# Kernel optimization log

Measured on AMD Instinct MI355X. Metric: run time of the kernel, lower is better.

Reference implementation:

```python
import jax, jax.numpy as jnp
import numpy as np

B, N, C, H = 4, 1024, 1024, 16
HD = C // H
SCALE = HD ** -0.5


def _init_linear(key, out_dim, in_dim):
    # torch nn.Linear default init: U(-1/sqrt(in), 1/sqrt(in)) for weight and bias
    kw, kb = jax.random.split(key)
    bound = 1.0 / np.sqrt(in_dim)
    W = jax.random.uniform(kw, (out_dim, in_dim), jnp.float32, -bound, bound)
    b = jax.random.uniform(kb, (out_dim,), jnp.float32, -bound, bound)
    return W, b


def setup_inputs() -> dict:
    key = jax.random.key(0)
    ks = jax.random.split(key, 5)
    x = jax.random.normal(ks[0], (B, N, C), jnp.float32)
    # NdLinear qkv: Linear(N->N) along seq axis, then Linear(C->3C) along channel axis
    Wq0, bq0 = _init_linear(ks[1], N, N)
    Wq1, bq1 = _init_linear(ks[2], 3 * C, C)
    # NdLinear proj: Linear(N->N) along seq axis, then Linear(C->C) along channel axis
    Wp0, bp0 = _init_linear(ks[3], N, N)
    Wp1, bp1 = _init_linear(ks[4], C, C)
    return {"x": x, "Wq0": Wq0, "bq0": bq0, "Wq1": Wq1, "bq1": bq1,
            "Wp0": Wp0, "bp0": bp0, "Wp1": Wp1, "bp1": bp1}


def _ndlinear(x, W0, b0, W1, b1):
    # NdLinear over (seq, channel): apply Linear along axis 1, then axis 2.
    # torch Linear: y = x @ W.T + b
    x = jnp.einsum('bnc,mn->bmc', x, W0) + b0[None, :, None]   # seq axis
    x = jnp.einsum('bnc,dc->bnd', x, W1) + b1                  # channel axis
    return x


def reference(x, Wq0, bq0, Wq1, bq1, Wp0, bp0, Wp1, bp1):
    qkv = _ndlinear(x, Wq0, bq0, Wq1, bq1)                     # (B, N, 3C)
    qkv = qkv.reshape(B, N, 3, H, HD).transpose(2, 0, 3, 1, 4) # (3, B, H, N, HD)
    q, k, v = qkv[0], qkv[1], qkv[2]
    attn = jnp.einsum('bhnd,bhmd->bhnm', q, k) * SCALE         # (B, H, N, N)
    attn = jax.nn.softmax(attn, axis=-1)
    out = jnp.einsum('bhnm,bhmd->bhnd', attn, v)               # (B, H, N, HD)
    out = out.transpose(0, 2, 1, 3).reshape(B, N, C)
    out = _ndlinear(out, Wp0, bp0, Wp1, bp1)
    return out
```

## Files before the change

kernel.cpp:

```cpp
#include <hip/hip_runtime.h>
#include <hip/hip_bf16.h>
#include <stdint.h>

typedef __bf16 bf16;
typedef __bf16 bf16x4 __attribute__((ext_vector_type(4)));
typedef __bf16 bf16x8 __attribute__((ext_vector_type(8)));
typedef float f32x4 __attribute__((ext_vector_type(4)));

#define B_ 4
#define N_ 1024
#define C_ 1024
#define H_ 16
#define MEG (1u << 20)

__device__ __forceinline__ uint32_t lds_off(const void* p) {
    return (uint32_t)(uintptr_t)p;
}
__device__ __forceinline__ void g2l16(const void* g, uint32_t lds_byte) {
    __builtin_amdgcn_global_load_lds(
        (const __attribute__((address_space(1))) unsigned int*)(uintptr_t)g,
        (__attribute__((address_space(3))) unsigned int*)(uintptr_t)lds_byte,
        16, 0, 0);
}

__global__ __launch_bounds__(256) void prep_k(
    const float* __restrict__ x, bf16* __restrict__ xT,
    const float* __restrict__ s0, bf16* __restrict__ d0,
    const float* __restrict__ s1, bf16* __restrict__ d1,
    const float* __restrict__ s2, bf16* __restrict__ d2,
    const float* __restrict__ s3, bf16* __restrict__ d3)
{
    __shared__ bf16 t[64][66];
    const int bid = blockIdx.x;
    const int tid = threadIdx.x;
    if (bid < 3072) {
        const float* s; bf16* d; int base;
        if (bid < 512)       { s = s0; d = d0; base = 0; }
        else if (bid < 2048) { s = s1; d = d1; base = 512; }
        else if (bid < 2560) { s = s2; d = d2; base = 2048; }
        else                 { s = s3; d = d3; base = 2560; }
        int i = ((bid - base) * 256 + tid) * 8;
        float4 a = *(const float4*)(s + i);
        float4 b = *(const float4*)(s + i + 4);
        bf16x8 r;
        r[0] = (bf16)a.x; r[1] = (bf16)a.y; r[2] = (bf16)a.z; r[3] = (bf16)a.w;
        r[4] = (bf16)b.x; r[5] = (bf16)b.y; r[6] = (bf16)b.z; r[7] = (bf16)b.w;
        *(bf16x8*)(d + i) = r;
        return;
    }
    const int idx = bid - 3072;
    const int c0 = (idx & 15) * 64, n0 = ((idx >> 4) & 15) * 64, b = idx >> 8;
    {
        int nl = tid >> 2, seg = tid & 3;
        const float* src = x + ((size_t)b * N_ + n0 + nl) * C_ + c0 + seg * 16;
#pragma unroll
        for (int i = 0; i < 4; ++i) {
            float4 v = *(const float4*)(src + i * 4);
            t[nl][seg * 16 + i * 4 + 0] = (bf16)v.x;
            t[nl][seg * 16 + i * 4 + 1] = (bf16)v.y;
            t[nl][seg * 16 + i * 4 + 2] = (bf16)v.z;
            t[nl][seg * 16 + i * 4 + 3] = (bf16)v.w;
        }
    }
    __syncthreads();
    {
        int cl = tid >> 2, seg = tid & 3;
        bf16* dst = xT + ((size_t)b * C_ + c0 + cl) * N_ + n0 + seg * 16;
        bf16x8 o0, o1;
#pragma unroll
        for (int j = 0; j < 8; ++j) o0[j] = t[seg * 16 + j][cl];
#pragma unroll
        for (int j = 0; j < 8; ++j) o1[j] = t[seg * 16 + 8 + j][cl];
        *(bf16x8*)dst = o0;
        *(bf16x8*)(dst + 8) = o1;
    }
}

template <int BIAS, bool OF32, bool VSPLIT>
__global__ __launch_bounds__(512) void gemm_k(
    const bf16* __restrict__ A, const bf16* __restrict__ Bm,
    const float* __restrict__ bias, void* __restrict__ Cv,
    bf16* __restrict__ vT,
    int M, int Nn, int K, long long sA, long long sB, long long sC)
{
    __shared__ bf16 smem[2][2][128 * 64];

    const int tid = threadIdx.x;
    const int lane = tid & 63, wid = tid >> 6;
    const int lr = lane & 15, lg = lane >> 4;
    const int wr = wid >> 2, wc = wid & 3;
    const int m0 = blockIdx.y * 128, n0 = blockIdx.x * 128;

    const bf16* Ab = A + (size_t)blockIdx.z * sA;
    const bf16* Bb = Bm + (size_t)blockIdx.z * sB;

    const uint32_t a_lds0 = lds_off(&smem[0][0][0]);
    const uint32_t b_lds0 = lds_off(&smem[0][1][0]);
    const uint32_t bufstride = 2 * 128 * 64 * 2;

    auto stage = [&](int kt, int buf) {
#pragma unroll
        for (int half = 0; half < 2; ++half) {
            int it = tid + half * 512;
            int r = it >> 3, ch = it & 7;
            int sch = ch ^ (r & 7);
            g2l16(Ab + (size_t)(m0 + r) * K + kt * 64 + sch * 8,
                  a_lds0 + buf * bufstride + it * 16);
            g2l16(Bb + (size_t)(n0 + r) * K + kt * 64 + sch * 8,
                  b_lds0 + buf * bufstride + it * 16);
        }
    };

    f32x4 acc[4][2];
#pragma unroll
    for (int i = 0; i < 4; ++i)
#pragma unroll
        for (int j = 0; j < 2; ++j) { f32x4 z = {0.f,0.f,0.f,0.f}; acc[i][j] = z; }

    stage(0, 0);
    __syncthreads();

    const int nt = K >> 6;
    for (int t = 0; t < nt; ++t) {
        int buf = t & 1;
        if (t + 1 < nt) stage(t + 1, buf ^ 1);
        const bf16* As = &smem[buf][0][0];
        const bf16* Bs = &smem[buf][1][0];
#pragma unroll
        for (int s = 0; s < 2; ++s) {
            bf16x8 af[4], bfr[2];
#pragma unroll
            for (int mi = 0; mi < 4; ++mi) {
                int row = wr * 64 + mi * 16 + lr;
                int slot = (s * 4 + lg) ^ (row & 7);
                af[mi] = *(const bf16x8*)(As + row * 64 + slot * 8);
            }
#pragma unroll
            for (int ni = 0; ni < 2; ++ni) {
                int row = wc * 32 + ni * 16 + lr;
                int slot = (s * 4 + lg) ^ (row & 7);
                bfr[ni] = *(const bf16x8*)(Bs + row * 64 + slot * 8);
            }
#pragma unroll
            for (int mi = 0; mi < 4; ++mi)
#pragma unroll
                for (int ni = 0; ni < 2; ++ni)
                    acc[mi][ni] = __builtin_amdgcn_mfma_f32_16x16x32_bf16(
                        af[mi], bfr[ni], acc[mi][ni], 0, 0, 0);
        }
        __syncthreads();
    }

#pragma unroll
    for (int mi = 0; mi < 4; ++mi)
#pragma unroll
        for (int ni = 0; ni < 2; ++ni) {
            int col = n0 + wc * 32 + ni * 16 + lr;
            if constexpr (VSPLIT) {
                if (col >= 2048) {
                    float bv = bias[col];
                    bf16x4 w;
#pragma unroll
                    for (int r = 0; r < 4; ++r) w[r] = (bf16)(acc[mi][ni][r] + bv);
                    int row0 = m0 + wr * 64 + mi * 16 + lg * 4;
                    int bb = row0 >> 10, n = row0 & 1023;
                    *(bf16x4*)(vT + (size_t)bb * MEG +
                               (size_t)(col - 2048) * 1024 + n) = w;
                    continue;
                }
            }
#pragma unroll
            for (int r = 0; r < 4; ++r) {
                int row = m0 + wr * 64 + mi * 16 + lg * 4 + r;
                float bv = (BIAS == 0) ? bias[row] : bias[col];
                float v = acc[mi][ni][r] + bv;
                if constexpr (OF32)
                    ((float*)Cv + (size_t)blockIdx.z * sC)[(size_t)row * Nn + col] = v;
                else
                    ((bf16*)Cv + (size_t)blockIdx.z * sC)[(size_t)row * Nn + col] = (bf16)v;
            }
        }
}

template <int BIAS, bool OF32>
__global__ __launch_bounds__(256) void gemm64_k(
    const bf16* __restrict__ A, const bf16* __restrict__ Bm,
    const float* __restrict__ bias, void* __restrict__ Cv,
    int M, int Nn, int K, long long sA, long long sB, long long sC)
{
    __shared__ bf16 smem[2][192 * 64];

    const int tid = threadIdx.x;
    const int lane = tid & 63, wid = tid >> 6;
    const int lr = lane & 15, lg = lane >> 4;
    const int wr = wid >> 1, wc = wid & 1;
    const int m0 = blockIdx.y * 128, n0 = blockIdx.x * 64;

    const bf16* Ab = A + (size_t)blockIdx.z * sA;
    const bf16* Bb = Bm + (size_t)blockIdx.z * sB;

    const uint32_t a_lds0 = lds_off(&smem[0][0]);
    const uint32_t b_lds0 = a_lds0 + 128 * 64 * 2;
    const uint32_t bufstride = 192 * 64 * 2;

    auto stage = [&](int kt, int buf) {
#pragma unroll
        for (int h = 0; h < 4; ++h) {
            int it = tid + h * 256;
            int r = it >> 3, ch = it & 7;
            int sch = ch ^ (r & 7);
            g2l16(Ab + (size_t)(m0 + r) * K + kt * 64 + sch * 8,
                  a_lds0 + buf * bufstride + it * 16);
        }
#pragma unroll
        for (int h = 0; h < 2; ++h) {
            int it = tid + h * 256;
            int r = it >> 3, ch = it & 7;
            int sch = ch ^ (r & 7);
            g2l16(Bb + (size_t)(n0 + r) * K + kt * 64 + sch * 8,
                  b_lds0 + buf * bufstride + it * 16);
        }
    };

    f32x4 acc[4][2];
#pragma unroll
    for (int i = 0; i < 4; ++i)
#pragma unroll
        for (int j = 0; j < 2; ++j) { f32x4 z = {0.f,0.f,0.f,0.f}; acc[i][j] = z; }

    stage(0, 0);
    __syncthreads();

    const int nt = K >> 6;
    for (int t = 0; t < nt; ++t) {
        int buf = t & 1;
        if (t + 1 < nt) stage(t + 1, buf ^ 1);
        const bf16* As = &smem[buf][0];
        const bf16* Bs = &smem[buf][128 * 64];
#pragma unroll
        for (int s = 0; s < 2; ++s) {
            bf16x8 af[4], bfr[2];
#pragma unroll
            for (int mi = 0; mi < 4; ++mi) {
                int row = wr * 64 + mi * 16 + lr;
                int slot = (s * 4 + lg) ^ (row & 7);
                af[mi] = *(const bf16x8*)(As + row * 64 + slot * 8);
            }
#pragma unroll
            for (int ni = 0; ni < 2; ++ni) {
                int row = wc * 32 + ni * 16 + lr;
                int slot = (s * 4 + lg) ^ (row & 7);
                bfr[ni] = *(const bf16x8*)(Bs + row * 64 + slot * 8);
            }
#pragma unroll
            for (int mi = 0; mi < 4; ++mi)
#pragma unroll
                for (int ni = 0; ni < 2; ++ni)
                    acc[mi][ni] = __builtin_amdgcn_mfma_f32_16x16x32_bf16(
                        af[mi], bfr[ni], acc[mi][ni], 0, 0, 0);
        }
        __syncthreads();
    }

#pragma unroll
    for (int mi = 0; mi < 4; ++mi)
#pragma unroll
        for (int ni = 0; ni < 2; ++ni)
#pragma unroll
            for (int r = 0; r < 4; ++r) {
                int row = m0 + wr * 64 + mi * 16 + lg * 4 + r;
                int col = n0 + wc * 32 + ni * 16 + lr;
                float bv = (BIAS == 0) ? bias[row] : bias[col];
                float v = acc[mi][ni][r] + bv;
                if constexpr (OF32)
                    ((float*)Cv + (size_t)blockIdx.z * sC)[(size_t)row * Nn + col] = v;
                else
                    ((bf16*)Cv + (size_t)blockIdx.z * sC)[(size_t)row * Nn + col] = (bf16)v;
            }
}

__global__ __launch_bounds__(256) void attn_k(
    const bf16* __restrict__ qkv, const bf16* __restrict__ vT,
    bf16* __restrict__ aoT)
{
    __shared__ bf16 Ks[2][4096];
    __shared__ bf16 Vs[2][4096];
    __shared__ bf16 pbuf[4][2048];

    const int tid = threadIdx.x;
    const int lane = tid & 63, wid = tid >> 6;
    const int lr = lane & 15, lg = lane >> 4;
    const int bid = blockIdx.x;
    const int qt = bid >> 6, hb = bid & 63;
    const int b = hb >> 4, h = hb & 15;
    const int qrow0 = qt * 128 + wid * 32;
    const int hoff = h * 64;
    const bf16* qkvb = qkv + (size_t)b * (N_ * 3 * C_);
    const bf16* vTb  = vT + (size_t)b * MEG;

    bf16x8 qfA[2], qfB[2];
#pragma unroll
    for (int kk = 0; kk < 2; ++kk) {
        qfA[kk] = *(const bf16x8*)(qkvb + (size_t)(qrow0 + lr) * 3072 +
                                   hoff + kk * 32 + lg * 8);
        qfB[kk] = *(const bf16x8*)(qkvb + (size_t)(qrow0 + 16 + lr) * 3072 +
                                   hoff + kk * 32 + lg * 8);
#pragma unroll
        for (int j = 0; j < 8; ++j) {
            qfA[kk][j] = (bf16)((float)qfA[kk][j] * 0.18033688f);
            qfB[kk][j] = (bf16)((float)qfB[kk][j] * 0.18033688f);
        }
    }

    const uint32_t ks0 = lds_off(&Ks[0][0]);
    const uint32_t vs0 = lds_off(&Vs[0][0]);

    auto stageK = [&](int kt, int buf) {
#pragma unroll
        for (int hh = 0; hh < 2; ++hh) {
            int it = tid + hh * 256;
            int key = it >> 3, ch = it & 7;
            int sch = ch ^ (key & 7);
            g2l16(qkvb + (size_t)(kt * 64 + key) * 3072 + C_ + hoff + sch * 8,
                  ks0 + buf * 8192 + it * 16);
        }
    };
    auto stageV = [&](int kt, int buf) {
#pragma unroll
        for (int hh = 0; hh < 2; ++hh) {
            int it = tid + hh * 256;
            int d = it >> 3, ch = it & 7;
            int sch = ch ^ (d & 7);
            g2l16(vTb + (size_t)(hoff + d) * 1024 + kt * 64 + sch * 8,
                  vs0 + buf * 8192 + it * 16);
        }
    };

    float lsumA = 0.f, lsumB = 0.f;
    f32x4 oA[4], oB[4];
#pragma unroll
    for (int i = 0; i < 4; ++i) {
        f32x4 z = {0.f,0.f,0.f,0.f};
        oA[i] = z; oB[i] = z;
    }

    char* prowA = (char*)&pbuf[wid][0] + lr * 128;
    char* prowB = (char*)&pbuf[wid][0] + (16 + lr) * 128;
    const int swz = (lr & 7) << 4;

    stageK(0, 0);
    stageV(0, 0);
    __syncthreads();

    for (int kt = 0; kt < 16; ++kt) {
        int buf = kt & 1;
        if (kt + 1 < 16) {
            stageK(kt + 1, buf ^ 1);
            stageV(kt + 1, buf ^ 1);
        }

        f32x4 sA[4], sB[4];
        __builtin_amdgcn_s_setprio(1);
#pragma unroll
        for (int st = 0; st < 4; ++st) {
            f32x4 zA = {0.f, 0.f, 0.f, 0.f};
            f32x4 zB = {0.f, 0.f, 0.f, 0.f};
#pragma unroll
            for (int kk = 0; kk < 2; ++kk) {
                int row = st * 16 + lr;
                int slot = (kk * 4 + lg) ^ (row & 7);
                bf16x8 kf = *(const bf16x8*)(&Ks[buf][row * 64 + slot * 8]);
                zA = __builtin_amdgcn_mfma_f32_16x16x32_bf16(kf, qfA[kk], zA, 0, 0, 0);
                zB = __builtin_amdgcn_mfma_f32_16x16x32_bf16(kf, qfB[kk], zB, 0, 0, 0);
            }
            sA[st] = zA; sB[st] = zB;
        }
        __builtin_amdgcn_s_setprio(0);

#pragma unroll
        for (int st = 0; st < 4; ++st) {
            bf16x4 wA, wB;
#pragma unroll
            for (int r = 0; r < 4; ++r) {
                float eA = __builtin_amdgcn_exp2f(sA[st][r]);
                float eB = __builtin_amdgcn_exp2f(sB[st][r]);
                wA[r] = (bf16)eA; lsumA += eA;
                wB[r] = (bf16)eB; lsumB += eB;
            }
            *(bf16x4*)(prowA + ((st * 32 + lg * 8) ^ swz)) = wA;
            *(bf16x4*)(prowB + ((st * 32 + lg * 8) ^ swz)) = wB;
        }

        bf16x8 pfA[2], pfB[2];
        pfA[0] = *(const bf16x8*)(prowA + ((lg * 16) ^ swz));
        pfA[1] = *(const bf16x8*)(prowA + ((64 + lg * 16) ^ swz));
        pfB[0] = *(const bf16x8*)(prowB + ((lg * 16) ^ swz));
        pfB[1] = *(const bf16x8*)(prowB + ((64 + lg * 16) ^ swz));

        __builtin_amdgcn_s_setprio(1);
#pragma unroll
        for (int dt = 0; dt < 4; ++dt) {
            int row = dt * 16 + lr;
            bf16x8 v0 = *(const bf16x8*)(&Vs[buf][row * 64 + ((lg ^ (lr & 7)) * 8)]);
            bf16x8 v1 = *(const bf16x8*)(&Vs[buf][row * 64 + (((4 + lg) ^ (lr & 7)) * 8)]);
            oA[dt] = __builtin_amdgcn_mfma_f32_16x16x32_bf16(pfA[0], v0, oA[dt], 0, 0, 0);
            oA[dt] = __builtin_amdgcn_mfma_f32_16x16x32_bf16(pfA[1], v1, oA[dt], 0, 0, 0);
            oB[dt] = __builtin_amdgcn_mfma_f32_16x16x32_bf16(pfB[0], v0, oB[dt], 0, 0, 0);
            oB[dt] = __builtin_amdgcn_mfma_f32_16x16x32_bf16(pfB[1], v1, oB[dt], 0, 0, 0);
        }
        __builtin_amdgcn_s_setprio(0);

        __syncthreads();
    }

    lsumA += __shfl_xor(lsumA, 16, 64);
    lsumA += __shfl_xor(lsumA, 32, 64);
    lsumB += __shfl_xor(lsumB, 16, 64);
    lsumB += __shfl_xor(lsumB, 32, 64);
    float rtotA = 1.0f / lsumA, rtotB = 1.0f / lsumB;
    float rcpoA[4], rcpoB[4];
#pragma unroll
    for (int r = 0; r < 4; ++r) {
        rcpoA[r] = __shfl(rtotA, lg * 4 + r, 64);
        rcpoB[r] = __shfl(rtotB, lg * 4 + r, 64);
    }

#pragma unroll
    for (int dt = 0; dt < 4; ++dt) {
        bf16x4 ovA, ovB;
#pragma unroll
        for (int r = 0; r < 4; ++r) {
            ovA[r] = (bf16)(oA[dt][r] * rcpoA[r]);
            ovB[r] = (bf16)(oB[dt][r] * rcpoB[r]);
        }
        size_t c = (size_t)b * C_ + hoff + dt * 16 + lr;
        *(bf16x4*)(aoT + c * N_ + qrow0 + lg * 4) = ovA;
        *(bf16x4*)(aoT + c * N_ + qrow0 + 16 + lg * 4) = ovB;
    }
}

extern "C" void kernel_launch(void* const* d_in, const int* in_sizes, int n_in,
                              void* d_out, int out_size, void* d_ws, size_t ws_size,
                              hipStream_t stream) {
    (void)in_sizes; (void)n_in; (void)out_size; (void)ws_size;
    const float* x   = (const float*)d_in[0];
    const float* Wq0 = (const float*)d_in[1];
    const float* bq0 = (const float*)d_in[2];
    const float* Wq1 = (const float*)d_in[3];
    const float* bq1 = (const float*)d_in[4];
    const float* Wp0 = (const float*)d_in[5];
    const float* bp0 = (const float*)d_in[6];
    const float* Wp1 = (const float*)d_in[7];
    const float* bp1 = (const float*)d_in[8];

    bf16* ws   = (bf16*)d_ws;
    bf16* xT   = ws;
    bf16* Wq0b = ws + 4 * MEG;
    bf16* Wq1b = ws + 5 * MEG;
    bf16* Wp0b = ws + 8 * MEG;
    bf16* Wp1b = ws + 9 * MEG;
    bf16* y1   = ws + 10 * MEG;
    bf16* y2   = ws + 14 * MEG;
    bf16* vT   = xT;
    bf16* aoT  = y1;
    bf16* z1   = y2;
    float* outp = (float*)d_out;

    const long long s1M = (long long)N_ * C_;

    prep_k<<<dim3(4096), 256, 0, stream>>>(x, xT, Wq0, Wq0b, Wq1, Wq1b,
                                           Wp0, Wp0b, Wp1, Wp1b);

    gemm64_k<0, false><<<dim3(16, 8, 4), 256, 0, stream>>>(
        Wq0b, xT, bq0, y1, 1024, 1024, 1024, 0LL, s1M, s1M);
    gemm_k<1, false, true><<<dim3(24, 32, 1), 512, 0, stream>>>(
        y1, Wq1b, bq1, y2, vT, 4096, 3072, 1024, 0LL, 0LL, 0LL);
    attn_k<<<dim3(512), 256, 0, stream>>>(y2, vT, aoT);
    gemm64_k<0, false><<<dim3(16, 8, 4), 256, 0, stream>>>(
        Wp0b, aoT, bp0, z1, 1024, 1024, 1024, 0LL, s1M, s1M);
    gemm64_k<1, true><<<dim3(16, 32, 1), 256, 0, stream>>>(
        z1, Wp1b, bp1, outp, 4096, 1024, 1024, 0LL, 0LL, 0LL);
}
```

Measured before the change: 116.3 us.

## Use 256x192 tiles with interleaved prefetch for the QKV channel GEMM

The QKV channel-projection GEMM moves from 128x128 tiles to 256x192 tiles, so each wave holds an 8x3 accumulator array. The grid becomes exactly 256 blocks, and each loaded byte is reused across more output. The next K-slice's loads are split across the four sub-steps, and explicit barriers, waitcnts and setprio are placed around the MFMA bursts so loads overlap compute. In exchange the kernel uses more LDS (112KB) and more registers, leaving one block per CU, and edge-case generality is lost.

```diff
diff --git a/kernel.cpp b/kernel.cpp
--- a/kernel.cpp
+++ b/kernel.cpp
@@ -77,92 +77,103 @@
 }
 
 template <int BIAS, bool OF32, bool VSPLIT>
-__global__ __launch_bounds__(512) void gemm_k(
+__global__ __launch_bounds__(512) void gemm256_k(
     const bf16* __restrict__ A, const bf16* __restrict__ Bm,
     const float* __restrict__ bias, void* __restrict__ Cv,
-    bf16* __restrict__ vT,
-    int M, int Nn, int K, long long sA, long long sB, long long sC)
+    bf16* __restrict__ vT, int M, int Nn, int K)
 {
-    __shared__ bf16 smem[2][2][128 * 64];
+    __shared__ bf16 smem[2 * 28672];
 
     const int tid = threadIdx.x;
     const int lane = tid & 63, wid = tid >> 6;
     const int lr = lane & 15, lg = lane >> 4;
-    const int wr = wid >> 2, wc = wid & 3;
-    const int m0 = blockIdx.y * 128, n0 = blockIdx.x * 128;
-
-    const bf16* Ab = A + (size_t)blockIdx.z * sA;
-    const bf16* Bb = Bm + (size_t)blockIdx.z * sB;
-
-    const uint32_t a_lds0 = lds_off(&smem[0][0][0]);
-    const uint32_t b_lds0 = lds_off(&smem[0][1][0]);
-    const uint32_t bufstride = 2 * 128 * 64 * 2;
-
-    auto stage = [&](int kt, int buf) {
-#pragma unroll
-        for (int half = 0; half < 2; ++half) {
-            int it = tid + half * 512;
-            int r = it >> 3, ch = it & 7;
+    const int wm = wid >> 2, wn = wid & 3;
+    const int m0 = blockIdx.y * 256, n0 = blockIdx.x * 192;
+
+    const uint32_t lds0 = lds_off(&smem[0]);
+
+    auto stageA = [&](int u) {
+        const uint32_t dst = lds0 + (u & 1) * 57344u;
+#pragma unroll
+        for (int hh = 0; hh < 4; ++hh) {
+            int c = tid + hh * 512;
+            int r = c >> 3, ch = c & 7;
             int sch = ch ^ (r & 7);
-            g2l16(Ab + (size_t)(m0 + r) * K + kt * 64 + sch * 8,
-                  a_lds0 + buf * bufstride + it * 16);
-            g2l16(Bb + (size_t)(n0 + r) * K + kt * 64 + sch * 8,
-                  b_lds0 + buf * bufstride + it * 16);
+            g2l16(A + (size_t)(m0 + r) * K + u * 64 + sch * 8, dst + c * 16u);
         }
     };
-
-    f32x4 acc[4][2];
-#pragma unroll
-    for (int i = 0; i < 4; ++i)
-#pragma unroll
-        for (int j = 0; j < 2; ++j) { f32x4 z = {0.f,0.f,0.f,0.f}; acc[i][j] = z; }
-
-    stage(0, 0);
-    __syncthreads();
+    auto stageB = [&](int u) {
+        const uint32_t dst = lds0 + (u & 1) * 57344u + 32768u;
+#pragma unroll
+        for (int hh = 0; hh < 3; ++hh) {
+            int c = tid + hh * 512;
+            int r = c >> 3, ch = c & 7;
+            int sch = ch ^ (r & 7);
+            g2l16(Bm + (size_t)(n0 + r) * K + u * 64 + sch * 8, dst + c * 16u);
+        }
+    };
+
+    f32x4 acc[8][3];
+#pragma unroll
+    for (int i = 0; i < 8; ++i)
+#pragma unroll
+        for (int j = 0; j < 3; ++j) { f32x4 z = {0.f,0.f,0.f,0.f}; acc[i][j] = z; }
+
+    stageA(0);
+    stageB(0);
+    asm volatile("s_waitcnt vmcnt(0)" ::: "memory");
+    __builtin_amdgcn_s_barrier();
 
     const int nt = K >> 6;
-    for (int t = 0; t < nt; ++t) {
-        int buf = t & 1;
-        if (t + 1 < nt) stage(t + 1, buf ^ 1);
-        const bf16* As = &smem[buf][0][0];
-        const bf16* Bs = &smem[buf][1][0];
-#pragma unroll
-        for (int s = 0; s < 2; ++s) {
-            bf16x8 af[4], bfr[2];
+    for (int u = 0; u < nt; ++u) {
+        const bf16* As = smem + (u & 1) * 28672;
+        const bf16* Bs = As + 16384;
+#pragma unroll
+        for (int q = 0; q < 4; ++q) {
+            const int mh = q >> 1, kk = q & 1;
+            bf16x8 af[4], bfr[3];
 #pragma unroll
             for (int mi = 0; mi < 4; ++mi) {
-                int row = wr * 64 + mi * 16 + lr;
-                int slot = (s * 4 + lg) ^ (row & 7);
+                int row = wm * 128 + mh * 64 + mi * 16 + lr;
+                int slot = (kk * 4 + lg) ^ (row & 7);
                 af[mi] = *(const bf16x8*)(As + row * 64 + slot * 8);
             }
 #pragma unroll
-            for (int ni = 0; ni < 2; ++ni) {
-                int row = wc * 32 + ni * 16 + lr;
-                int slot = (s * 4 + lg) ^ (row & 7);
+            for (int ni = 0; ni < 3; ++ni) {
+                int row = wn * 48 + ni * 16 + lr;
+                int slot = (kk * 4 + lg) ^ (row & 7);
                 bfr[ni] = *(const bf16x8*)(Bs + row * 64 + slot * 8);
             }
+            if (q == 0 && u + 1 < nt) stageA(u + 1);
+            if (q == 1 && u + 1 < nt) stageB(u + 1);
+            __builtin_amdgcn_s_barrier();
+            asm volatile("s_waitcnt lgkmcnt(0)" ::: "memory");
+            __builtin_amdgcn_s_setprio(1);
 #pragma unroll
             for (int mi = 0; mi < 4; ++mi)
 #pragma unroll
-                for (int ni = 0; ni < 2; ++ni)
-                    acc[mi][ni] = __builtin_amdgcn_mfma_f32_16x16x32_bf16(
-                        af[mi], bfr[ni], acc[mi][ni], 0, 0, 0);
-        }
-        __syncthreads();
-    }
-
-#pragma unroll
-    for (int mi = 0; mi < 4; ++mi)
-#pragma unroll
-        for (int ni = 0; ni < 2; ++ni) {
-            int col = n0 + wc * 32 + ni * 16 + lr;
+                for (int ni = 0; ni < 3; ++ni)
+                    acc[mh * 4 + mi][ni] = __builtin_amdgcn_mfma_f32_16x16x32_bf16(
+                        af[mi], bfr[ni], acc[mh * 4 + mi][ni], 0, 0, 0);
+            __builtin_amdgcn_s_setprio(0);
+            if (q == 3)
+                asm volatile("s_waitcnt vmcnt(0)" ::: "memory");
+            __builtin_amdgcn_s_barrier();
+        }
+    }
+
+#pragma unroll
+    for (int mi = 0; mi < 8; ++mi)
+#pragma unroll
+        for (int ni = 0; ni < 3; ++ni) {
+            int col = n0 + wn * 48 + ni * 16 + lr;
             if constexpr (VSPLIT) {
                 if (col >= 2048) {
                     float bv = bias[col];
                     bf16x4 w;
 #pragma unroll
                     for (int r = 0; r < 4; ++r) w[r] = (bf16)(acc[mi][ni][r] + bv);
-                    int row0 = m0 + wr * 64 + mi * 16 + lg * 4;
+                    int row0 = m0 + wm * 128 + mi * 16 + lg * 4;
                     int bb = row0 >> 10, n = row0 & 1023;
                     *(bf16x4*)(vT + (size_t)bb * MEG +
                                (size_t)(col - 2048) * 1024 + n) = w;
@@ -171,13 +182,13 @@
             }
 #pragma unroll
             for (int r = 0; r < 4; ++r) {
-                int row = m0 + wr * 64 + mi * 16 + lg * 4 + r;
+                int row = m0 + wm * 128 + mi * 16 + lg * 4 + r;
                 float bv = (BIAS == 0) ? bias[row] : bias[col];
                 float v = acc[mi][ni][r] + bv;
                 if constexpr (OF32)
-                    ((float*)Cv + (size_t)blockIdx.z * sC)[(size_t)row * Nn + col] = v;
+                    ((float*)Cv)[(size_t)row * Nn + col] = v;
                 else
-                    ((bf16*)Cv + (size_t)blockIdx.z * sC)[(size_t)row * Nn + col] = (bf16)v;
+                    ((bf16*)Cv)[(size_t)row * Nn + col] = (bf16)v;
             }
         }
 }
@@ -473,8 +484,8 @@
 
     gemm64_k<0, false><<<dim3(16, 8, 4), 256, 0, stream>>>(
         Wq0b, xT, bq0, y1, 1024, 1024, 1024, 0LL, s1M, s1M);
-    gemm_k<1, false, true><<<dim3(24, 32, 1), 512, 0, stream>>>(
-        y1, Wq1b, bq1, y2, vT, 4096, 3072, 1024, 0LL, 0LL, 0LL);
+    gemm256_k<1, false, true><<<dim3(16, 16), 512, 0, stream>>>(
+        y1, Wq1b, bq1, y2, vT, 4096, 3072, 1024);
     attn_k<<<dim3(512), 256, 0, stream>>>(y2, vT, aoT);
     gemm64_k<0, false><<<dim3(16, 8, 4), 256, 0, stream>>>(
         Wp0b, aoT, bp0, z1, 1024, 1024, 1024, 0LL, s1M, s1M);
```

After: 118.4 us. About the same (+1.9%).

## Software-pipeline attention: prefetch two tiles ahead and overlap QK^T with PV

Applied to the files above, without the earlier changes.

Restructures the attention key loop into a deeper software pipeline. K and V tiles are now prefetched two iterations ahead, with V triple-buffered in LDS. The next tile's QK^T MFMAs are issued before the current tile's PV MFMAs, and the __syncthreads calls become raw s_barrier plus explicit vmcnt waits. The aim is to hide global-load latency and interleave the softmax exp with matrix work. The cost is extra LDS for the third V buffer, more live registers for the next score tile, and reliance on hand-counted vmcnt values being correct.

```diff
diff --git a/kernel.cpp b/kernel.cpp
--- a/kernel.cpp
+++ b/kernel.cpp
@@ -284,7 +284,7 @@
     bf16* __restrict__ aoT)
 {
     __shared__ bf16 Ks[2][4096];
-    __shared__ bf16 Vs[2][4096];
+    __shared__ bf16 Vs[3][4096];
     __shared__ bf16 pbuf[4][2048];
 
     const int tid = threadIdx.x;
@@ -336,6 +336,26 @@
         }
     };
 
+    auto qkt = [&](int kt, f32x4* SA, f32x4* SB) {
+        const bf16* Kbase = &Ks[kt & 1][0];
+        __builtin_amdgcn_s_setprio(1);
+#pragma unroll
+        for (int st = 0; st < 4; ++st) {
+            f32x4 zA = {0.f, 0.f, 0.f, 0.f};
+            f32x4 zB = {0.f, 0.f, 0.f, 0.f};
+#pragma unroll
+            for (int kk = 0; kk < 2; ++kk) {
+                int row = st * 16 + lr;
+                int slot = (kk * 4 + lg) ^ (row & 7);
+                bf16x8 kf = *(const bf16x8*)(Kbase + row * 64 + slot * 8);
+                zA = __builtin_amdgcn_mfma_f32_16x16x32_bf16(kf, qfA[kk], zA, 0, 0, 0);
+                zB = __builtin_amdgcn_mfma_f32_16x16x32_bf16(kf, qfB[kk], zB, 0, 0, 0);
+            }
+            SA[st] = zA; SB[st] = zB;
+        }
+        __builtin_amdgcn_s_setprio(0);
+    };
+
     float lsumA = 0.f, lsumB = 0.f;
     f32x4 oA[4], oB[4];
 #pragma unroll
@@ -348,34 +368,20 @@
     char* prowB = (char*)&pbuf[wid][0] + (16 + lr) * 128;
     const int swz = (lr & 7) << 4;
 
-    stageK(0, 0);
-    stageV(0, 0);
-    __syncthreads();
+    stageK(0, 0); stageV(0, 0);
+    stageK(1, 1); stageV(1, 1);
+    asm volatile("s_waitcnt vmcnt(4)" ::: "memory");
+    __builtin_amdgcn_s_barrier();
+
+    f32x4 sA[4], sB[4];
+    qkt(0, sA, sB);
+    __builtin_amdgcn_s_barrier();
 
     for (int kt = 0; kt < 16; ++kt) {
-        int buf = kt & 1;
-        if (kt + 1 < 16) {
-            stageK(kt + 1, buf ^ 1);
-            stageV(kt + 1, buf ^ 1);
-        }
-
-        f32x4 sA[4], sB[4];
-        __builtin_amdgcn_s_setprio(1);
-#pragma unroll
-        for (int st = 0; st < 4; ++st) {
-            f32x4 zA = {0.f, 0.f, 0.f, 0.f};
-            f32x4 zB = {0.f, 0.f, 0.f, 0.f};
-#pragma unroll
-            for (int kk = 0; kk < 2; ++kk) {
-                int row = st * 16 + lr;
-                int slot = (kk * 4 + lg) ^ (row & 7);
-                bf16x8 kf = *(const bf16x8*)(&Ks[buf][row * 64 + slot * 8]);
-                zA = __builtin_amdgcn_mfma_f32_16x16x32_bf16(kf, qfA[kk], zA, 0, 0, 0);
-                zB = __builtin_amdgcn_mfma_f32_16x16x32_bf16(kf, qfB[kk], zB, 0, 0, 0);
-            }
-            sA[st] = zA; sB[st] = zB;
-        }
-        __builtin_amdgcn_s_setprio(0);
+        if (kt + 2 < 16) {
+            stageK(kt + 2, kt & 1);
+            stageV(kt + 2, (kt + 2) % 3);
+        }
 
 #pragma unroll
         for (int st = 0; st < 4; ++st) {
@@ -391,18 +397,29 @@
             *(bf16x4*)(prowB + ((st * 32 + lg * 8) ^ swz)) = wB;
         }
 
+        f32x4 nA[4], nB[4];
+        if (kt + 1 < 16) {
+            if (kt + 2 < 16)
+                asm volatile("s_waitcnt vmcnt(4)" ::: "memory");
+            else
+                asm volatile("s_waitcnt vmcnt(0)" ::: "memory");
+            __builtin_amdgcn_s_barrier();
+            qkt(kt + 1, nA, nB);
+        }
+
         bf16x8 pfA[2], pfB[2];
         pfA[0] = *(const bf16x8*)(prowA + ((lg * 16) ^ swz));
         pfA[1] = *(const bf16x8*)(prowA + ((64 + lg * 16) ^ swz));
         pfB[0] = *(const bf16x8*)(prowB + ((lg * 16) ^ swz));
         pfB[1] = *(const bf16x8*)(prowB + ((64 + lg * 16) ^ swz));
 
+        const bf16* Vbase = &Vs[kt % 3][0];
         __builtin_amdgcn_s_setprio(1);
 #pragma unroll
         for (int dt = 0; dt < 4; ++dt) {
             int row = dt * 16 + lr;
-            bf16x8 v0 = *(const bf16x8*)(&Vs[buf][row * 64 + ((lg ^ (lr & 7)) * 8)]);
-            bf16x8 v1 = *(const bf16x8*)(&Vs[buf][row * 64 + (((4 + lg) ^ (lr & 7)) * 8)]);
+            bf16x8 v0 = *(const bf16x8*)(Vbase + row * 64 + ((lg ^ (lr & 7)) * 8));
+            bf16x8 v1 = *(const bf16x8*)(Vbase + row * 64 + (((4 + lg) ^ (lr & 7)) * 8));
             oA[dt] = __builtin_amdgcn_mfma_f32_16x16x32_bf16(pfA[0], v0, oA[dt], 0, 0, 0);
             oA[dt] = __builtin_amdgcn_mfma_f32_16x16x32_bf16(pfA[1], v1, oA[dt], 0, 0, 0);
             oB[dt] = __builtin_amdgcn_mfma_f32_16x16x32_bf16(pfB[0], v0, oB[dt], 0, 0, 0);
@@ -410,7 +427,10 @@
         }
         __builtin_amdgcn_s_setprio(0);
 
-        __syncthreads();
+        __builtin_amdgcn_s_barrier();
+
+#pragma unroll
+        for (int i = 0; i < 4; ++i) { sA[i] = nA[i]; sB[i] = nB[i]; }
     }
 
     lsumA += __shfl_xor(lsumA, 16, 64);
```

Result: no change. 115.5 us, median of 4 (-0.7%).

## Load K/V tiles directly from global into registers instead of LDS staging

Applied to the files above, without the earlier changes.

The attention kernel no longer stages K and V tiles through double-buffered shared memory with async global-to-LDS copies and block barriers. Each wave now loads its K fragments straight into registers, with a manual two-tile software prefetch, and loads V fragments from global just before the PV MFMAs. This removes the per-tile __syncthreads and the LDS traffic. In exchange, each of the four waves in a block fetches the same K/V data from global/L2 separately, register pressure rises, and the V loads sit in the critical path without prefetch.

```diff
diff --git a/kernel.cpp b/kernel.cpp
--- a/kernel.cpp
+++ b/kernel.cpp
@@ -283,8 +283,6 @@
     const bf16* __restrict__ qkv, const bf16* __restrict__ vT,
     bf16* __restrict__ aoT)
 {
-    __shared__ bf16 Ks[2][4096];
-    __shared__ bf16 Vs[2][4096];
     __shared__ bf16 pbuf[4][2048];
 
     const int tid = threadIdx.x;
@@ -312,28 +310,16 @@
         }
     }
 
-    const uint32_t ks0 = lds_off(&Ks[0][0]);
-    const uint32_t vs0 = lds_off(&Vs[0][0]);
-
-    auto stageK = [&](int kt, int buf) {
-#pragma unroll
-        for (int hh = 0; hh < 2; ++hh) {
-            int it = tid + hh * 256;
-            int key = it >> 3, ch = it & 7;
-            int sch = ch ^ (key & 7);
-            g2l16(qkvb + (size_t)(kt * 64 + key) * 3072 + C_ + hoff + sch * 8,
-                  ks0 + buf * 8192 + it * 16);
-        }
-    };
-    auto stageV = [&](int kt, int buf) {
-#pragma unroll
-        for (int hh = 0; hh < 2; ++hh) {
-            int it = tid + hh * 256;
-            int d = it >> 3, ch = it & 7;
-            int sch = ch ^ (d & 7);
-            g2l16(vTb + (size_t)(hoff + d) * 1024 + kt * 64 + sch * 8,
-                  vs0 + buf * 8192 + it * 16);
-        }
+    const bf16* kbase = qkvb + (size_t)lr * 3072 + C_ + hoff + lg * 8;
+    const bf16* vbase = vTb + (size_t)(hoff + lr) * 1024 + lg * 8;
+
+    auto loadK = [&](int t, bf16x8 (&K)[4][2]) {
+#pragma unroll
+        for (int st = 0; st < 4; ++st)
+#pragma unroll
+            for (int kk = 0; kk < 2; ++kk)
+                K[st][kk] = *(const bf16x8*)(kbase +
+                    (size_t)(t * 64 + st * 16) * 3072 + kk * 32);
     };
 
     float lsumA = 0.f, lsumB = 0.f;
@@ -348,16 +334,14 @@
     char* prowB = (char*)&pbuf[wid][0] + (16 + lr) * 128;
     const int swz = (lr & 7) << 4;
 
-    stageK(0, 0);
-    stageV(0, 0);
-    __syncthreads();
-
-    for (int kt = 0; kt < 16; ++kt) {
-        int buf = kt & 1;
-        if (kt + 1 < 16) {
-            stageK(kt + 1, buf ^ 1);
-            stageV(kt + 1, buf ^ 1);
-        }
+    auto halfstep = [&](const bf16x8 (&K)[4][2], int t) {
+        bf16x8 Vv[4][2];
+#pragma unroll
+        for (int dt = 0; dt < 4; ++dt)
+#pragma unroll
+            for (int kk = 0; kk < 2; ++kk)
+                Vv[dt][kk] = *(const bf16x8*)(vbase +
+                    (size_t)(dt * 16) * 1024 + t * 64 + kk * 32);
 
         f32x4 sA[4], sB[4];
         __builtin_amdgcn_s_setprio(1);
@@ -367,11 +351,8 @@
             f32x4 zB = {0.f, 0.f, 0.f, 0.f};
 #pragma unroll
             for (int kk = 0; kk < 2; ++kk) {
-                int row = st * 16 + lr;
-                int slot = (kk * 4 + lg) ^ (row & 7);
-                bf16x8 kf = *(const bf16x8*)(&Ks[buf][row * 64 + slot * 8]);
-                zA = __builtin_amdgcn_mfma_f32_16x16x32_bf16(kf, qfA[kk], zA, 0, 0, 0);
-                zB = __builtin_amdgcn_mfma_f32_16x16x32_bf16(kf, qfB[kk], zB, 0, 0, 0);
+                zA = __builtin_amdgcn_mfma_f32_16x16x32_bf16(K[st][kk], qfA[kk], zA, 0, 0, 0);
+                zB = __builtin_amdgcn_mfma_f32_16x16x32_bf16(K[st][kk], qfB[kk], zB, 0, 0, 0);
             }
             sA[st] = zA; sB[st] = zB;
         }
@@ -400,17 +381,21 @@
         __builtin_amdgcn_s_setprio(1);
 #pragma unroll
         for (int dt = 0; dt < 4; ++dt) {
-            int row = dt * 16 + lr;
-            bf16x8 v0 = *(const bf16x8*)(&Vs[buf][row * 64 + ((lg ^ (lr & 7)) * 8)]);
-            bf16x8 v1 = *(const bf16x8*)(&Vs[buf][row * 64 + (((4 + lg) ^ (lr & 7)) * 8)]);
-            oA[dt] = __builtin_amdgcn_mfma_f32_16x16x32_bf16(pfA[0], v0, oA[dt], 0, 0, 0);
-            oA[dt] = __builtin_amdgcn_mfma_f32_16x16x32_bf16(pfA[1], v1, oA[dt], 0, 0, 0);
-            oB[dt] = __builtin_amdgcn_mfma_f32_16x16x32_bf16(pfB[0], v0, oB[dt], 0, 0, 0);
-            oB[dt] = __builtin_amdgcn_mfma_f32_16x16x32_bf16(pfB[1], v1, oB[dt], 0, 0, 0);
+            oA[dt] = __builtin_amdgcn_mfma_f32_16x16x32_bf16(pfA[0], Vv[dt][0], oA[dt], 0, 0, 0);
+            oA[dt] = __builtin_amdgcn_mfma_f32_16x16x32_bf16(pfA[1], Vv[dt][1], oA[dt], 0, 0, 0);
+            oB[dt] = __builtin_amdgcn_mfma_f32_16x16x32_bf16(pfB[0], Vv[dt][0], oB[dt], 0, 0, 0);
+            oB[dt] = __builtin_amdgcn_mfma_f32_16x16x32_bf16(pfB[1], Vv[dt][1], oB[dt], 0, 0, 0);
         }
         __builtin_amdgcn_s_setprio(0);
-
-        __syncthreads();
+    };
+
+    bf16x8 K0[4][2], K1[4][2];
+    loadK(0, K0);
+    for (int t = 0; t < 16; t += 2) {
+        loadK(t + 1, K1);
+        halfstep(K0, t);
+        if (t + 2 < 16) loadK(t + 2, K0);
+        halfstep(K1, t + 1);
     }
 
     lsumA += __shfl_xor(lsumA, 16, 64);
```

New measurement: 149.9 us. 28.9% more time.
